# Optimization experiments

Hardware: AMD Instinct MI355X
Metric: run time of the kernel (lower is better)

## Reference

```python
import jax, jax.numpy as jnp
import numpy as np
from jax import lax

B, IMG, CIN, C, HEADS, K = 2, 112, 64, 256, 8, 3  # kernel_size[0]=3 used by hatt1
HD = C // HEADS


def layer_norm(x, w, b, eps=1e-5):
    mu = jnp.mean(x, axis=-1, keepdims=True)
    var = jnp.mean((x - mu) ** 2, axis=-1, keepdims=True)
    return (x - mu) / jnp.sqrt(var + eps) * w + b


def conv3x3(x, w, b):
    # x: (B,Cin,H,W), w: (Cout,Cin,3,3) -- stride 1, pad 1 (OverlapPatchEmbed patchsize=3)
    y = lax.conv_general_dilated(x, w, (1, 1), ((1, 1), (1, 1)),
                                 dimension_numbers=('NCHW', 'OIHW', 'NCHW'))
    return y + b[None, :, None, None]


def nat_cross_attention(q_in, kv_in, wq, bq, wkv, bkv, rpb, wp, bp, heads=HEADS, k=K):
    # NATTEN-style 2D neighborhood attention with separate query / key-value maps.
    Bb, H, W, Cc = q_in.shape
    hd = Cc // heads
    scale = hd ** -0.5
    q = (q_in @ wq + bq).reshape(Bb, H, W, heads, hd) * scale
    kv = (kv_in @ wkv + bkv).reshape(Bb, H, W, 2, heads, hd)
    kk, v = kv[:, :, :, 0], kv[:, :, :, 1]
    half = k // 2
    # border-clamped window starts -> every pixel attends to a full k x k window
    si = jnp.clip(jnp.arange(H) - half, 0, H - k)  # (H,)
    sj = jnp.clip(jnp.arange(W) - half, 0, W - k)  # (W,)
    nbi = si[:, None] + jnp.arange(k)  # (H,k) neighbor rows
    nbj = sj[:, None] + jnp.arange(k)  # (W,k) neighbor cols

    def gather(t):  # t: (B,H,W,heads,hd) -> (B,H,W,heads,k*k,hd)
        g = t[:, nbi]            # (B,H,k,W,heads,hd)
        g = g[:, :, :, nbj]      # (B,H,k,W,k,heads,hd)
        return jnp.transpose(g, (0, 1, 3, 5, 2, 4, 6)).reshape(Bb, H, W, heads, k * k, hd)

    kg, vg = gather(kk), gather(v)
    logits = jnp.einsum('bijhd,bijhnd->bijhn', q, kg)
    # relative position bias: rpb (heads, 2k-1, 2k-1)
    pi = jnp.arange(H) - si  # query position inside its window, 0..k-1
    pj = jnp.arange(W) - sj
    idx_i = jnp.arange(k)[None, :] - pi[:, None] + (k - 1)  # (H,k) in [0, 2k-2]
    idx_j = jnp.arange(k)[None, :] - pj[:, None] + (k - 1)  # (W,k)
    bias = rpb[:, idx_i]           # (heads,H,k,2k-1)
    bias = bias[:, :, :, idx_j]    # (heads,H,k,W,k)
    bias = jnp.transpose(bias, (1, 3, 0, 2, 4)).reshape(H, W, heads, k * k)
    attn = jax.nn.softmax(logits + bias, axis=-1)
    out = jnp.einsum('bijhn,bijhnd->bijhd', attn, vg).reshape(Bb, H, W, Cc)
    return out @ wp + bp


def setup_inputs() -> dict:
    key = jax.random.key(0)
    ks = jax.random.split(key, 24)
    std = 0.02
    inp = {
        'xq': jax.random.normal(ks[0], (B, CIN, IMG, IMG), jnp.float32),
        'xkv': jax.random.normal(ks[1], (B, CIN, IMG, IMG), jnp.float32),
        'conv1_w': jax.random.normal(ks[2], (C, CIN, 3, 3), jnp.float32) * std,
        'conv1_b': jnp.zeros((C,), jnp.float32),
        'conv3_w': jax.random.normal(ks[3], (C, CIN, 3, 3), jnp.float32) * std,
        'conv3_b': jnp.zeros((C,), jnp.float32),
        'ln1_w': jnp.ones((C,), jnp.float32), 'ln1_b': jnp.zeros((C,), jnp.float32),
        'ln10_w': jnp.ones((C,), jnp.float32), 'ln10_b': jnp.zeros((C,), jnp.float32),
        'ln3_w': jnp.ones((C,), jnp.float32), 'ln3_b': jnp.zeros((C,), jnp.float32),
        'wq': jax.random.normal(ks[4], (C, C), jnp.float32) * std,
        'bq': jnp.zeros((C,), jnp.float32),
        'wkv': jax.random.normal(ks[5], (C, 2 * C), jnp.float32) * std,
        'bkv': jnp.zeros((2 * C,), jnp.float32),
        'rpb': jax.random.normal(ks[6], (HEADS, 2 * K - 1, 2 * K - 1), jnp.float32) * std,
        'wp': jax.random.normal(ks[7], (C, C), jnp.float32) * std,
        'bp': jnp.zeros((C,), jnp.float32),
        'fc1_w': jax.random.normal(ks[8], (C, 2 * C), jnp.float32) * std,
        'fc1_b': jnp.zeros((2 * C,), jnp.float32),
        'fc2_w': jax.random.normal(ks[9], (2 * C, C), jnp.float32) * std,
        'fc2_b': jnp.zeros((C,), jnp.float32),
    }
    return inp


def reference(xq, xkv, conv1_w, conv1_b, conv3_w, conv3_b, ln1_w, ln1_b, ln10_w, ln10_b,
              ln3_w, ln3_b, wq, bq, wkv, bkv, rpb, wp, bp, fc1_w, fc1_b, fc2_w, fc2_b):
    # patch embeds (stride-1 3x3 conv, pad 1), channels-last maps (B,H,W,C)
    x1 = jnp.transpose(conv3x3(xq, conv1_w, conv1_b), (0, 2, 3, 1))
    x3 = jnp.transpose(conv3x3(xkv, conv3_w, conv3_b), (0, 2, 3, 1))
    qn = layer_norm(x1, ln1_w, ln1_b)    # norm1(x_embedding1)
    kvn = layer_norm(x1, ln10_w, ln10_b)  # norm1_0(x_embedding1)
    att1 = nat_cross_attention(qn, kvn, wq, bq, wkv, bkv, rpb, wp, bp)
    att = att1 + x3  # drop_path is identity at inference
    h = layer_norm(att, ln3_w, ln3_b)
    m = jax.nn.gelu(h @ fc1_w + fc1_b, approximate=False) @ fc2_w + fc2_b
    x = m + att
    return jnp.transpose(x, (0, 3, 1, 2))  # (B,C,H,W)
```

## Files before the change

### kernel.cpp

```cpp
#include <hip/hip_runtime.h>
#include <math.h>

#define IMG 112
#define CIN 64
#define CH 256
#define PADW 114
#define IMG2 12544
#define NPIX 25088

typedef __bf16 bf16;
typedef __bf16 bf16x4 __attribute__((ext_vector_type(4)));
typedef __bf16 bf16x8 __attribute__((ext_vector_type(8)));
typedef float f32x4 __attribute__((ext_vector_type(4)));

__device__ __forceinline__ void gld_lds16(const void* g, void* l) {
    __builtin_amdgcn_global_load_lds(
        (const __attribute__((address_space(1))) void*)g,
        (__attribute__((address_space(3))) void*)l,
        16, 0, 0);
}

#define VMCNT0() asm volatile("s_waitcnt vmcnt(0)" ::: "memory")
#define BAR() __builtin_amdgcn_s_barrier()

__global__ __launch_bounds__(256) void pad_nhwc_kernel(const float* __restrict__ in, bf16* __restrict__ out) {
    int bi = blockIdx.x;
    int b = bi / IMG, i = bi % IMG;
    __shared__ float lds[CIN * 113];
    const float* src = in + (size_t)b * CIN * IMG2 + (size_t)i * IMG;
    for (int t = threadIdx.x; t < CIN * IMG; t += 256) {
        int ci = t / IMG, j = t - ci * IMG;
        lds[ci * 113 + j] = src[(size_t)ci * IMG2 + j];
    }
    __syncthreads();
    bf16* dst = out + (((size_t)(b * PADW + (i + 1)) * PADW) + 1) * CIN;
    for (int t = threadIdx.x; t < CIN * IMG; t += 256) {
        int j = t / CIN, ci = t - j * CIN;
        dst[(size_t)j * CIN + ci] = (bf16)lds[ci * 113 + j];
    }
}

__global__ __launch_bounds__(256) void convw_kernel(const float* __restrict__ w1, const float* __restrict__ w2,
                                                    bf16* __restrict__ o1, bf16* __restrict__ o2) {
    int idx = blockIdx.x * 256 + threadIdx.x;
    if (idx >= CH * 576) return;
    int co = idx / 576, r = idx - co * 576;
    int tap = r >> 6, ci = r & 63;
    int src = co * 576 + ci * 9 + tap;
    o1[idx] = (bf16)w1[src];
    o2[idx] = (bf16)w2[src];
}

__global__ __launch_bounds__(256) void transw_kernel(const float* __restrict__ in, bf16* __restrict__ out,
                                                     int K, int N, float scale) {
    int idx = blockIdx.x * 256 + threadIdx.x;
    if (idx >= N * K) return;
    int n = idx / K, k = idx - n * K;
    out[idx] = (bf16)(in[(size_t)k * N + n] * scale);
}

template <int NOUT>
__global__ __launch_bounds__(256) void ln_kernel(
    const float* __restrict__ x,
    const float* __restrict__ w0, const float* __restrict__ b0, bf16* __restrict__ o0,
    const float* __restrict__ w1, const float* __restrict__ b1, bf16* __restrict__ o1) {
    int row = blockIdx.x * 4 + (threadIdx.x >> 6);
    int lane = threadIdx.x & 63;
    const float* xr = x + (size_t)row * CH + lane * 4;
    f32x4 v = *(const f32x4*)xr;
    float s = v[0] + v[1] + v[2] + v[3];
    float ss = v[0] * v[0] + v[1] * v[1] + v[2] * v[2] + v[3] * v[3];
#pragma unroll
    for (int off = 32; off > 0; off >>= 1) {
        s += __shfl_xor(s, off);
        ss += __shfl_xor(ss, off);
    }
    float mean = s * (1.0f / CH);
    float rstd = rsqrtf(ss * (1.0f / CH) - mean * mean + 1e-5f);
    int c = lane * 4;
    {
        f32x4 w = *(const f32x4*)(w0 + c);
        f32x4 bb = *(const f32x4*)(b0 + c);
        bf16x4 o;
#pragma unroll
        for (int e = 0; e < 4; ++e) o[e] = (bf16)((v[e] - mean) * rstd * w[e] + bb[e]);
        *(bf16x4*)(o0 + (size_t)row * CH + c) = o;
    }
    if (NOUT == 2) {
        f32x4 w = *(const f32x4*)(w1 + c);
        f32x4 bb = *(const f32x4*)(b1 + c);
        bf16x4 o;
#pragma unroll
        for (int e = 0; e < 4; ++e) o[e] = (bf16)((v[e] - mean) * rstd * w[e] + bb[e]);
        *(bf16x4*)(o1 + (size_t)row * CH + c) = o;
    }
}

template <int AMODE, int EPI>
__global__ __launch_bounds__(256, 5) void gemm_kernel(
    const bf16* __restrict__ A, const bf16* __restrict__ Bt,
    const float* __restrict__ bias, float biasScale,
    const float* __restrict__ res,
    float* __restrict__ outf, bf16* __restrict__ outb,
    int N, int K) {
    __shared__ __align__(16) bf16 As[2][64 * 64];
    __shared__ __align__(16) bf16 Bs[2][64 * 64];
    const int tid = threadIdx.x;
    const int wave = tid >> 6, lane = tid & 63;
    const int m0 = blockIdx.x * 64, n0 = blockIdx.y * 64;
    const int wm = wave >> 1, wn = wave & 1;
    const int fr = lane & 15, fq = lane >> 4;

    const int srow = (lane >> 3);
    const int swzc = (lane & 7) ^ srow;
    const int scol = swzc * 8;

    const bf16* aptr[2];
    const bf16* bptr[2];
#pragma unroll
    for (int q = 0; q < 2; ++q) {
        int arow = m0 + wave * 16 + q * 8 + srow;
        if (AMODE == 1) {
            int b = arow / IMG2;
            int rem = arow - b * IMG2;
            int i = rem / IMG, j = rem - i * IMG;
            aptr[q] = A + ((size_t)((b * PADW + i) * PADW + j)) * CIN + scol;
        } else {
            aptr[q] = A + (size_t)arow * K + scol;
        }
        bptr[q] = Bt + (size_t)(n0 + wave * 16 + q * 8 + srow) * K + scol;
    }

    auto STAGE = [&](int bufi, int kt) {
        int aoff;
        if (AMODE == 1) {
            int di = kt / 3, dj = kt - di * 3;
            aoff = (di * PADW + dj) * CIN;
        } else {
            aoff = kt * 64;
        }
        int boff = kt * 64;
        gld_lds16(aptr[0] + aoff, &As[bufi][(wave * 16 + 0) * 64]);
        gld_lds16(aptr[1] + aoff, &As[bufi][(wave * 16 + 8) * 64]);
        gld_lds16(bptr[0] + boff, &Bs[bufi][(wave * 16 + 0) * 64]);
        gld_lds16(bptr[1] + boff, &Bs[bufi][(wave * 16 + 8) * 64]);
    };

    f32x4 acc[2][2] = {};
    const int sw = fr & 7;
    const int aR[2] = { (wm * 32 + fr) * 64, (wm * 32 + 16 + fr) * 64 };
    const int bR[2] = { (wn * 32 + fr) * 64, (wn * 32 + 16 + fr) * 64 };

    auto COMPUTE = [&](int bufi) {
#pragma unroll
        for (int ks = 0; ks < 2; ++ks) {
            int ch = (ks * 4 + fq) ^ sw;
            bf16x8 af[2], bv[2];
#pragma unroll
            for (int mi = 0; mi < 2; ++mi) af[mi] = *(const bf16x8*)&As[bufi][aR[mi] + ch * 8];
#pragma unroll
            for (int ni = 0; ni < 2; ++ni) bv[ni] = *(const bf16x8*)&Bs[bufi][bR[ni] + ch * 8];
#pragma unroll
            for (int mi = 0; mi < 2; ++mi)
#pragma unroll
                for (int ni = 0; ni < 2; ++ni)
                    acc[mi][ni] = __builtin_amdgcn_mfma_f32_16x16x32_bf16(af[mi], bv[ni], acc[mi][ni], 0, 0, 0);
        }
    };

    const int nk = K >> 6;
    STAGE(0, 0);
    VMCNT0();
    BAR();
    int cur = 0;
    for (int kt = 0; kt < nk - 1; ++kt) {
        STAGE(cur ^ 1, kt + 1);
        COMPUTE(cur);
        VMCNT0();
        BAR();
        cur ^= 1;
    }
    COMPUTE(cur);

#pragma unroll
    for (int mi = 0; mi < 2; ++mi) {
#pragma unroll
        for (int ni = 0; ni < 2; ++ni) {
            int col = n0 + wn * 32 + ni * 16 + fr;
            float bv = (EPI & 1) ? bias[col] * biasScale : 0.0f;
#pragma unroll
            for (int r = 0; r < 4; ++r) {
                int prow = m0 + wm * 32 + mi * 16 + fq * 4 + r;
                float x = acc[mi][ni][r] + bv;
                if (EPI & 2) x = 0.5f * x * (1.0f + erff(x * 0.70710678118f));
                if (EPI & 4) x += res[(size_t)prow * N + col];
                if (EPI & 8) outf[(size_t)prow * N + col] = x;
                if (EPI & 16) outb[(size_t)prow * N + col] = (bf16)x;
                if (EPI & 32) {
                    int b = prow / IMG2;
                    int rem = prow - b * IMG2;
                    int ii = rem / IMG, jj = rem - ii * IMG;
                    outf[(((size_t)b * CH + col) * IMG + ii) * IMG + jj] = x;
                }
            }
        }
    }
}

__global__ __launch_bounds__(256) void attn_kernel(const bf16* __restrict__ q, const bf16* __restrict__ kv,
                                                   const float* __restrict__ rpb, bf16* __restrict__ out) {
    int idx = blockIdx.x * 256 + threadIdx.x;
    int h = idx & 7, p = idx >> 3;
    int b = p / IMG2;
    int rem = p - b * IMG2;
    int i = rem / IMG, j = rem - i * IMG;
    int si = i - 1; if (si < 0) si = 0; if (si > IMG - 3) si = IMG - 3;
    int sj = j - 1; if (sj < 0) sj = 0; if (sj > IMG - 3) sj = IMG - 3;
    int pi = i - si, pj = j - sj;

    float qv[32];
    {
        const bf16x8* qp = (const bf16x8*)(q + (size_t)p * CH + h * 32);
#pragma unroll
        for (int g = 0; g < 4; ++g) {
            bf16x8 t = qp[g];
#pragma unroll
            for (int e = 0; e < 8; ++e) qv[g * 8 + e] = (float)t[e];
        }
    }
    float logits[9];
#pragma unroll
    for (int a = 0; a < 3; ++a) {
#pragma unroll
        for (int bb = 0; bb < 3; ++bb) {
            int pn = (b * IMG + (si + a)) * IMG + (sj + bb);
            const bf16x8* kp = (const bf16x8*)(kv + (size_t)pn * 512 + h * 32);
            float s = 0.0f;
#pragma unroll
            for (int g = 0; g < 4; ++g) {
                bf16x8 t = kp[g];
#pragma unroll
                for (int e = 0; e < 8; ++e) s += qv[g * 8 + e] * (float)t[e];
            }
            logits[a * 3 + bb] = s + rpb[(h * 5 + (a - pi + 2)) * 5 + (bb - pj + 2)];
        }
    }
    float mx = logits[0];
#pragma unroll
    for (int n = 1; n < 9; ++n) mx = fmaxf(mx, logits[n]);
    float den = 0.0f;
#pragma unroll
    for (int n = 0; n < 9; ++n) { logits[n] = expf(logits[n] - mx); den += logits[n]; }
    float inv = 1.0f / den;
    float o[32] = {};
#pragma unroll
    for (int a = 0; a < 3; ++a) {
#pragma unroll
        for (int bb = 0; bb < 3; ++bb) {
            int pn = (b * IMG + (si + a)) * IMG + (sj + bb);
            float wgt = logits[a * 3 + bb] * inv;
            const bf16x8* vp = (const bf16x8*)(kv + (size_t)pn * 512 + 256 + h * 32);
#pragma unroll
            for (int g = 0; g < 4; ++g) {
                bf16x8 t = vp[g];
#pragma unroll
                for (int e = 0; e < 8; ++e) o[g * 8 + e] += wgt * (float)t[e];
            }
        }
    }
    bf16* op = out + (size_t)p * CH + h * 32;
#pragma unroll
    for (int g = 0; g < 4; ++g) {
        bf16x8 t;
#pragma unroll
        for (int e = 0; e < 8; ++e) t[e] = (bf16)o[g * 8 + e];
        *(bf16x8*)(op + g * 8) = t;
    }
}

extern "C" void kernel_launch(void* const* d_in, const int* in_sizes, int n_in,
                              void* d_out, int out_size, void* d_ws, size_t ws_size,
                              hipStream_t stream) {
    (void)in_sizes; (void)n_in; (void)out_size; (void)ws_size;
    const float* xq    = (const float*)d_in[0];
    const float* xkv   = (const float*)d_in[1];
    const float* c1w   = (const float*)d_in[2];
    const float* c1b   = (const float*)d_in[3];
    const float* c3w   = (const float*)d_in[4];
    const float* c3b   = (const float*)d_in[5];
    const float* ln1w  = (const float*)d_in[6];
    const float* ln1b  = (const float*)d_in[7];
    const float* ln10w = (const float*)d_in[8];
    const float* ln10b = (const float*)d_in[9];
    const float* ln3w  = (const float*)d_in[10];
    const float* ln3b  = (const float*)d_in[11];
    const float* wq    = (const float*)d_in[12];
    const float* bq    = (const float*)d_in[13];
    const float* wkv   = (const float*)d_in[14];
    const float* bkv   = (const float*)d_in[15];
    const float* rpb   = (const float*)d_in[16];
    const float* wp    = (const float*)d_in[17];
    const float* bp    = (const float*)d_in[18];
    const float* f1w   = (const float*)d_in[19];
    const float* f1b   = (const float*)d_in[20];
    const float* f2w   = (const float*)d_in[21];
    const float* f2b   = (const float*)d_in[22];
    float* out = (float*)d_out;

    char* ws = (char*)d_ws;
    bf16*  PADQ  = (bf16*)(ws + 0);
    bf16*  PADKV = (bf16*)(ws + 3326976);
    bf16*  CW1   = (bf16*)(ws + 6653952);
    bf16*  CW2   = (bf16*)(ws + 6948864);
    bf16*  WQT   = (bf16*)(ws + 7243776);
    bf16*  WKVT  = (bf16*)(ws + 7374848);
    bf16*  WPT   = (bf16*)(ws + 7636992);
    bf16*  WF1   = (bf16*)(ws + 7768064);
    bf16*  WF2   = (bf16*)(ws + 8030208);
    float* X1    = (float*)(ws + 8292352);
    bf16*  KV    = (bf16*)(ws + 8292352);
    float* X3    = (float*)(ws + 33982464);
    bf16*  QN    = (bf16*)(ws + 59672576);
    bf16*  M1    = (bf16*)(ws + 59672576);
    bf16*  KVN   = (bf16*)(ws + 72517632);
    bf16*  Q     = (bf16*)(ws + 85362688);
    bf16*  H     = (bf16*)(ws + 85362688);
    bf16*  AO    = (bf16*)(ws + 98207744);
    float* ATT   = (float*)(ws + 111052800);

    const float SC = 0.17677669529663687f;

    hipMemsetAsync(PADQ, 0, 6653952, stream);
    pad_nhwc_kernel<<<224, 256, 0, stream>>>(xq, PADQ);
    pad_nhwc_kernel<<<224, 256, 0, stream>>>(xkv, PADKV);
    convw_kernel<<<576, 256, 0, stream>>>(c1w, c3w, CW1, CW2);
    transw_kernel<<<256, 256, 0, stream>>>(wq, WQT, 256, 256, SC);
    transw_kernel<<<512, 256, 0, stream>>>(wkv, WKVT, 256, 512, 1.0f);
    transw_kernel<<<256, 256, 0, stream>>>(wp, WPT, 256, 256, 1.0f);
    transw_kernel<<<512, 256, 0, stream>>>(f1w, WF1, 256, 512, 1.0f);
    transw_kernel<<<512, 256, 0, stream>>>(f2w, WF2, 512, 256, 1.0f);

    dim3 g4(392, 4), g8(392, 8);
    gemm_kernel<1, 1 | 8><<<g4, 256, 0, stream>>>(PADQ, CW1, c1b, 1.0f, nullptr, X1, nullptr, 256, 576);
    gemm_kernel<1, 1 | 8><<<g4, 256, 0, stream>>>(PADKV, CW2, c3b, 1.0f, nullptr, X3, nullptr, 256, 576);
    ln_kernel<2><<<6272, 256, 0, stream>>>(X1, ln1w, ln1b, QN, ln10w, ln10b, KVN);
    gemm_kernel<0, 1 | 16><<<g4, 256, 0, stream>>>(QN, WQT, bq, SC, nullptr, nullptr, Q, 256, 256);
    gemm_kernel<0, 1 | 16><<<g8, 256, 0, stream>>>(KVN, WKVT, bkv, 1.0f, nullptr, nullptr, KV, 512, 256);
    attn_kernel<<<784, 256, 0, stream>>>(Q, KV, rpb, AO);
    gemm_kernel<0, 1 | 4 | 8><<<g4, 256, 0, stream>>>(AO, WPT, bp, 1.0f, X3, ATT, nullptr, 256, 256);
    ln_kernel<1><<<6272, 256, 0, stream>>>(ATT, ln3w, ln3b, H, nullptr, nullptr, nullptr);
    gemm_kernel<0, 1 | 2 | 16><<<g8, 256, 0, stream>>>(H, WF1, f1b, 1.0f, nullptr, nullptr, M1, 512, 256);
    gemm_kernel<0, 1 | 4 | 32><<<g4, 256, 0, stream>>>(M1, WF2, f2b, 1.0f, ATT, out, nullptr, 256, 512);
}
```

Before: 298.3 us.

## Fuse prep kernels, widen GEMM tiles to full rows, fold LayerNorms into GEMM epilogues

All weight and input prep launches are merged into a single kernel, and the memset is replaced by writing only the padding borders. The GEMM now computes 64x256 tiles so each block holds full channel rows, which lets both LayerNorms run in the epilogues through LDS row reductions, and the NCHW output is written with vectorized stores through an LDS transpose. Intermediate activations such as X3 and ATT are stored in bf16 instead of fp32, cutting memory traffic but adding rounding error. The change removes several launches and full fp32 round trips, but the larger tile uses 80KB LDS per block and needs more accumulator registers, which lowers occupancy.

```diff
diff --git a/kernel.cpp b/kernel.cpp
--- a/kernel.cpp
+++ b/kernel.cpp
@@ -7,9 +7,9 @@
 #define PADW 114
 #define IMG2 12544
 #define NPIX 25088
+#define SCQ 0.17677669529663687f
 
 typedef __bf16 bf16;
-typedef __bf16 bf16x4 __attribute__((ext_vector_type(4)));
 typedef __bf16 bf16x8 __attribute__((ext_vector_type(8)));
 typedef float f32x4 __attribute__((ext_vector_type(4)));
 
@@ -19,104 +19,97 @@
         (__attribute__((address_space(3))) void*)l,
         16, 0, 0);
 }
-
 #define VMCNT0() asm volatile("s_waitcnt vmcnt(0)" ::: "memory")
 #define BAR() __builtin_amdgcn_s_barrier()
 
-__global__ __launch_bounds__(256) void pad_nhwc_kernel(const float* __restrict__ in, bf16* __restrict__ out) {
-    int bi = blockIdx.x;
-    int b = bi / IMG, i = bi % IMG;
+__global__ __launch_bounds__(256) void prep_kernel(
+    const float* __restrict__ xq, const float* __restrict__ xkv,
+    bf16* __restrict__ padq, bf16* __restrict__ padkv,
+    const float* __restrict__ c1w, const float* __restrict__ c3w,
+    bf16* __restrict__ cw1, bf16* __restrict__ cw2,
+    const float* __restrict__ wq, bf16* __restrict__ wqt,
+    const float* __restrict__ wkv, bf16* __restrict__ wkvt,
+    const float* __restrict__ wp, bf16* __restrict__ wpt,
+    const float* __restrict__ f1w, bf16* __restrict__ wf1,
+    const float* __restrict__ f2w, bf16* __restrict__ wf2) {
+    int bid = blockIdx.x, tid = threadIdx.x;
     __shared__ float lds[CIN * 113];
-    const float* src = in + (size_t)b * CIN * IMG2 + (size_t)i * IMG;
-    for (int t = threadIdx.x; t < CIN * IMG; t += 256) {
-        int ci = t / IMG, j = t - ci * IMG;
-        lds[ci * 113 + j] = src[(size_t)ci * IMG2 + j];
-    }
-    __syncthreads();
-    bf16* dst = out + (((size_t)(b * PADW + (i + 1)) * PADW) + 1) * CIN;
-    for (int t = threadIdx.x; t < CIN * IMG; t += 256) {
-        int j = t / CIN, ci = t - j * CIN;
-        dst[(size_t)j * CIN + ci] = (bf16)lds[ci * 113 + j];
-    }
-}
-
-__global__ __launch_bounds__(256) void convw_kernel(const float* __restrict__ w1, const float* __restrict__ w2,
-                                                    bf16* __restrict__ o1, bf16* __restrict__ o2) {
-    int idx = blockIdx.x * 256 + threadIdx.x;
-    if (idx >= CH * 576) return;
-    int co = idx / 576, r = idx - co * 576;
-    int tap = r >> 6, ci = r & 63;
-    int src = co * 576 + ci * 9 + tap;
-    o1[idx] = (bf16)w1[src];
-    o2[idx] = (bf16)w2[src];
-}
-
-__global__ __launch_bounds__(256) void transw_kernel(const float* __restrict__ in, bf16* __restrict__ out,
-                                                     int K, int N, float scale) {
-    int idx = blockIdx.x * 256 + threadIdx.x;
-    if (idx >= N * K) return;
-    int n = idx / K, k = idx - n * K;
-    out[idx] = (bf16)(in[(size_t)k * N + n] * scale);
-}
-
-template <int NOUT>
-__global__ __launch_bounds__(256) void ln_kernel(
-    const float* __restrict__ x,
-    const float* __restrict__ w0, const float* __restrict__ b0, bf16* __restrict__ o0,
-    const float* __restrict__ w1, const float* __restrict__ b1, bf16* __restrict__ o1) {
-    int row = blockIdx.x * 4 + (threadIdx.x >> 6);
-    int lane = threadIdx.x & 63;
-    const float* xr = x + (size_t)row * CH + lane * 4;
-    f32x4 v = *(const f32x4*)xr;
-    float s = v[0] + v[1] + v[2] + v[3];
-    float ss = v[0] * v[0] + v[1] * v[1] + v[2] * v[2] + v[3] * v[3];
-#pragma unroll
-    for (int off = 32; off > 0; off >>= 1) {
-        s += __shfl_xor(s, off);
-        ss += __shfl_xor(ss, off);
-    }
-    float mean = s * (1.0f / CH);
-    float rstd = rsqrtf(ss * (1.0f / CH) - mean * mean + 1e-5f);
-    int c = lane * 4;
-    {
-        f32x4 w = *(const f32x4*)(w0 + c);
-        f32x4 bb = *(const f32x4*)(b0 + c);
-        bf16x4 o;
-#pragma unroll
-        for (int e = 0; e < 4; ++e) o[e] = (bf16)((v[e] - mean) * rstd * w[e] + bb[e]);
-        *(bf16x4*)(o0 + (size_t)row * CH + c) = o;
-    }
-    if (NOUT == 2) {
-        f32x4 w = *(const f32x4*)(w1 + c);
-        f32x4 bb = *(const f32x4*)(b1 + c);
-        bf16x4 o;
-#pragma unroll
-        for (int e = 0; e < 4; ++e) o[e] = (bf16)((v[e] - mean) * rstd * w[e] + bb[e]);
-        *(bf16x4*)(o1 + (size_t)row * CH + c) = o;
-    }
-}
-
-template <int AMODE, int EPI>
-__global__ __launch_bounds__(256, 5) void gemm_kernel(
-    const bf16* __restrict__ A, const bf16* __restrict__ Bt,
-    const float* __restrict__ bias, float biasScale,
-    const float* __restrict__ res,
-    float* __restrict__ outf, bf16* __restrict__ outb,
-    int N, int K) {
-    __shared__ __align__(16) bf16 As[2][64 * 64];
-    __shared__ __align__(16) bf16 Bs[2][64 * 64];
+    if (bid < 448) {
+        const float* in = (bid < 224) ? xq : xkv;
+        bf16* out = (bid < 224) ? padq : padkv;
+        int bi = (bid < 224) ? bid : bid - 224;
+        int b = bi / IMG, i = bi % IMG;
+        const float* src = in + (size_t)b * CIN * IMG2 + (size_t)i * IMG;
+        for (int t = tid; t < CIN * IMG; t += 256) {
+            int ci = t / IMG, j = t - ci * IMG;
+            lds[ci * 113 + j] = src[(size_t)ci * IMG2 + j];
+        }
+        __syncthreads();
+        bf16* dst = out + (((size_t)(b * PADW + (i + 1)) * PADW) + 1) * CIN;
+        for (int t = tid; t < CIN * IMG; t += 256) {
+            int j = t / CIN, ci = t - j * CIN;
+            dst[(size_t)j * CIN + ci] = (bf16)lds[ci * 113 + j];
+        }
+        bf16* rowbase = out + ((size_t)(b * PADW + (i + 1)) * PADW) * CIN;
+        if (tid < 128) rowbase[(tid >> 6 ? 113 * CIN : 0) + (tid & 63)] = (bf16)0.0f;
+        if (i == 0)
+            for (int t = tid; t < PADW * CIN; t += 256)
+                out[((size_t)(b * PADW + 0) * PADW) * CIN + t] = (bf16)0.0f;
+        if (i == IMG - 1)
+            for (int t = tid; t < PADW * CIN; t += 256)
+                out[((size_t)(b * PADW + 113) * PADW) * CIN + t] = (bf16)0.0f;
+    } else if (bid < 1024) {
+        int idx = (bid - 448) * 256 + tid;
+        int co = idx / 576, r = idx - co * 576;
+        int tap = r >> 6, ci = r & 63;
+        int src = co * 576 + ci * 9 + tap;
+        cw1[idx] = (bf16)c1w[src];
+        cw2[idx] = (bf16)c3w[src];
+    } else {
+        int off = (bid - 1024) * 256 + tid;
+        const float* in; bf16* out; int K, N; float sc = 1.0f; int base;
+        if (off < 65536)       { in = wq;  out = wqt;  K = 256; N = 256; sc = SCQ; base = 0; }
+        else if (off < 196608) { in = wkv; out = wkvt; K = 256; N = 512; base = 65536; }
+        else if (off < 262144) { in = wp;  out = wpt;  K = 256; N = 256; base = 196608; }
+        else if (off < 393216) { in = f1w; out = wf1;  K = 256; N = 512; base = 262144; }
+        else                   { in = f2w; out = wf2;  K = 512; N = 256; base = 393216; }
+        int idx = off - base;
+        int n = idx / K, k = idx - n * K;
+        out[idx] = (bf16)(in[(size_t)k * N + n] * sc);
+    }
+}
+
+#define M_DENSE 0
+#define M_LN2   1
+#define M_WPLN  2
+#define M_GELU  3
+#define M_NCHW  4
+
+template <int AMODE, int MODE>
+__device__ __forceinline__ void gemm_core(
+    char* sm,
+    const bf16* __restrict__ A, const bf16* __restrict__ B,
+    const float* __restrict__ bias, float bscale,
+    const bf16* __restrict__ res,
+    bf16* __restrict__ out0, int ldo0,
+    bf16* __restrict__ out1, float* __restrict__ outf,
+    const float* __restrict__ lnw0, const float* __restrict__ lnb0,
+    const float* __restrict__ lnw1, const float* __restrict__ lnb1,
+    int K) {
+    bf16* As = (bf16*)sm;
+    bf16* Bs = (bf16*)(sm + 16384);
+    float* lnb = (float*)sm;
+    float* T = (float*)(sm + 2048);
+
     const int tid = threadIdx.x;
     const int wave = tid >> 6, lane = tid & 63;
-    const int m0 = blockIdx.x * 64, n0 = blockIdx.y * 64;
+    const int m0 = blockIdx.x * 64;
     const int wm = wave >> 1, wn = wave & 1;
     const int fr = lane & 15, fq = lane >> 4;
-
-    const int srow = (lane >> 3);
-    const int swzc = (lane & 7) ^ srow;
-    const int scol = swzc * 8;
+    const int srow = lane >> 3;
+    const int scol = ((lane & 7) ^ srow) * 8;
 
     const bf16* aptr[2];
-    const bf16* bptr[2];
 #pragma unroll
     for (int q = 0; q < 2; ++q) {
         int arow = m0 + wave * 16 + q * 8 + srow;
@@ -128,42 +121,38 @@
         } else {
             aptr[q] = A + (size_t)arow * K + scol;
         }
-        bptr[q] = Bt + (size_t)(n0 + wave * 16 + q * 8 + srow) * K + scol;
-    }
-
-    auto STAGE = [&](int bufi, int kt) {
-        int aoff;
-        if (AMODE == 1) {
-            int di = kt / 3, dj = kt - di * 3;
-            aoff = (di * PADW + dj) * CIN;
-        } else {
-            aoff = kt * 64;
-        }
+    }
+    const bf16* bptr0 = B + (size_t)(wave * 64 + srow) * K + scol;
+
+    auto STAGE = [&](int bi, int kt) {
+        int aoff = (AMODE == 1) ? ((kt / 3) * PADW + (kt - (kt / 3) * 3)) * CIN : kt * 64;
         int boff = kt * 64;
-        gld_lds16(aptr[0] + aoff, &As[bufi][(wave * 16 + 0) * 64]);
-        gld_lds16(aptr[1] + aoff, &As[bufi][(wave * 16 + 8) * 64]);
-        gld_lds16(bptr[0] + boff, &Bs[bufi][(wave * 16 + 0) * 64]);
-        gld_lds16(bptr[1] + boff, &Bs[bufi][(wave * 16 + 8) * 64]);
+        bf16* ad = As + bi * 4096 + (wave * 16) * 64;
+        gld_lds16(aptr[0] + aoff, ad);
+        gld_lds16(aptr[1] + aoff, ad + 8 * 64);
+        bf16* bd = Bs + bi * 16384 + (wave * 64) * 64;
+#pragma unroll
+        for (int u = 0; u < 8; ++u)
+            gld_lds16(bptr0 + (size_t)u * 8 * K + boff, bd + u * 8 * 64);
     };
 
-    f32x4 acc[2][2] = {};
-    const int sw = fr & 7;
-    const int aR[2] = { (wm * 32 + fr) * 64, (wm * 32 + 16 + fr) * 64 };
-    const int bR[2] = { (wn * 32 + fr) * 64, (wn * 32 + 16 + fr) * 64 };
-
-    auto COMPUTE = [&](int bufi) {
+    f32x4 acc[2][8] = {};
+    auto COMPUTE = [&](int bi) {
+        const bf16* ab = As + bi * 4096;
+        const bf16* bb = Bs + bi * 16384;
 #pragma unroll
         for (int ks = 0; ks < 2; ++ks) {
-            int ch = (ks * 4 + fq) ^ sw;
-            bf16x8 af[2], bv[2];
-#pragma unroll
-            for (int mi = 0; mi < 2; ++mi) af[mi] = *(const bf16x8*)&As[bufi][aR[mi] + ch * 8];
-#pragma unroll
-            for (int ni = 0; ni < 2; ++ni) bv[ni] = *(const bf16x8*)&Bs[bufi][bR[ni] + ch * 8];
+            int ch = ((ks * 4 + fq) ^ (fr & 7)) * 8;
+            bf16x8 af[2];
+#pragma unroll
+            for (int mi = 0; mi < 2; ++mi) af[mi] = *(const bf16x8*)&ab[(wm * 32 + mi * 16 + fr) * 64 + ch];
+            bf16x8 bv[8];
+#pragma unroll
+            for (int ni = 0; ni < 8; ++ni) bv[ni] = *(const bf16x8*)&bb[(wn * 128 + ni * 16 + fr) * 64 + ch];
 #pragma unroll
             for (int mi = 0; mi < 2; ++mi)
 #pragma unroll
-                for (int ni = 0; ni < 2; ++ni)
+                for (int ni = 0; ni < 8; ++ni)
                     acc[mi][ni] = __builtin_amdgcn_mfma_f32_16x16x32_bf16(af[mi], bv[ni], acc[mi][ni], 0, 0, 0);
         }
     };
@@ -182,29 +171,196 @@
     }
     COMPUTE(cur);
 
-#pragma unroll
-    for (int mi = 0; mi < 2; ++mi) {
-#pragma unroll
-        for (int ni = 0; ni < 2; ++ni) {
-            int col = n0 + wn * 32 + ni * 16 + fr;
-            float bv = (EPI & 1) ? bias[col] * biasScale : 0.0f;
+    float bvv[8];
+#pragma unroll
+    for (int ni = 0; ni < 8; ++ni) bvv[ni] = bias[wn * 128 + ni * 16 + fr] * bscale;
+#pragma unroll
+    for (int mi = 0; mi < 2; ++mi)
+#pragma unroll
+        for (int ni = 0; ni < 8; ++ni)
 #pragma unroll
             for (int r = 0; r < 4; ++r) {
-                int prow = m0 + wm * 32 + mi * 16 + fq * 4 + r;
-                float x = acc[mi][ni][r] + bv;
-                if (EPI & 2) x = 0.5f * x * (1.0f + erff(x * 0.70710678118f));
-                if (EPI & 4) x += res[(size_t)prow * N + col];
-                if (EPI & 8) outf[(size_t)prow * N + col] = x;
-                if (EPI & 16) outb[(size_t)prow * N + col] = (bf16)x;
-                if (EPI & 32) {
-                    int b = prow / IMG2;
-                    int rem = prow - b * IMG2;
-                    int ii = rem / IMG, jj = rem - ii * IMG;
-                    outf[(((size_t)b * CH + col) * IMG + ii) * IMG + jj] = x;
-                }
-            }
-        }
-    }
+                float x = acc[mi][ni][r] + bvv[ni];
+                if (MODE == M_WPLN) {
+                    int prow = m0 + wm * 32 + mi * 16 + fq * 4 + r;
+                    int col = wn * 128 + ni * 16 + fr;
+                    x += (float)res[(size_t)prow * 256 + col];
+                }
+                if (MODE == M_GELU) x = 0.5f * x * (1.0f + erff(x * 0.70710678118f));
+                acc[mi][ni][r] = x;
+            }
+
+    float mean_[2][4], rstd_[2][4];
+    if (MODE == M_LN2 || MODE == M_WPLN) {
+        BAR();
+#pragma unroll
+        for (int mi = 0; mi < 2; ++mi)
+#pragma unroll
+            for (int r = 0; r < 4; ++r) {
+                float s = 0.0f, ss = 0.0f;
+#pragma unroll
+                for (int ni = 0; ni < 8; ++ni) {
+                    float x = acc[mi][ni][r];
+                    s += x; ss += x * x;
+                }
+#pragma unroll
+                for (int msk = 1; msk <= 8; msk <<= 1) {
+                    s += __shfl_xor(s, msk);
+                    ss += __shfl_xor(ss, msk);
+                }
+                if (fr == 0) {
+                    int row = wm * 32 + mi * 16 + fq * 4 + r;
+                    lnb[wn * 128 + row] = s;
+                    lnb[wn * 128 + 64 + row] = ss;
+                }
+            }
+        BAR();
+#pragma unroll
+        for (int mi = 0; mi < 2; ++mi)
+#pragma unroll
+            for (int r = 0; r < 4; ++r) {
+                int row = wm * 32 + mi * 16 + fq * 4 + r;
+                float s = lnb[row] + lnb[128 + row];
+                float ss = lnb[64 + row] + lnb[192 + row];
+                float mean = s * (1.0f / CH);
+                float var = ss * (1.0f / CH) - mean * mean;
+                mean_[mi][r] = mean;
+                rstd_[mi][r] = rsqrtf(var + 1e-5f);
+            }
+    } else {
+        BAR();
+    }
+
+#pragma unroll
+    for (int mi = 0; mi < 2; ++mi)
+#pragma unroll
+        for (int ni = 0; ni < 8; ++ni)
+#pragma unroll
+            for (int r = 0; r < 4; ++r) {
+                int row = wm * 32 + mi * 16 + fq * 4 + r;
+                int col = wn * 128 + ni * 16 + fr;
+                float x = acc[mi][ni][r];
+                if (MODE == M_LN2) x = (x - mean_[mi][r]) * rstd_[mi][r];
+                T[row * 257 + col] = x;
+            }
+    BAR();
+
+    if (MODE == M_NCHW) {
+        int c = tid;
+        int b = m0 / IMG2, p0 = m0 - b * IMG2;
+        float* outp = outf + ((size_t)(b * CH + c)) * IMG2 + p0;
+        const bf16* rp = res + (size_t)m0 * 256 + c;
+#pragma unroll
+        for (int g = 0; g < 16; ++g) {
+            f32x4 v;
+#pragma unroll
+            for (int e = 0; e < 4; ++e)
+                v[e] = T[(g * 4 + e) * 257 + c] + (float)rp[(size_t)(g * 4 + e) * 256];
+            *(f32x4*)(outp + g * 4) = v;
+        }
+    } else {
+        int row = tid & 63, qd = tid >> 6;
+        int cb = qd * 64;
+        if (MODE == M_DENSE || MODE == M_GELU) {
+            bf16* op = out0 + (size_t)(m0 + row) * ldo0 + cb;
+#pragma unroll
+            for (int g = 0; g < 8; ++g) {
+                bf16x8 o;
+#pragma unroll
+                for (int e = 0; e < 8; ++e) o[e] = (bf16)T[row * 257 + cb + g * 8 + e];
+                *(bf16x8*)(op + g * 8) = o;
+            }
+        } else if (MODE == M_LN2) {
+            bf16* op0 = out0 + (size_t)(m0 + row) * 256 + cb;
+            bf16* op1 = out1 + (size_t)(m0 + row) * 256 + cb;
+#pragma unroll
+            for (int g = 0; g < 8; ++g) {
+                bf16x8 o0, o1;
+#pragma unroll
+                for (int e = 0; e < 8; ++e) {
+                    int c = cb + g * 8 + e;
+                    float xh = T[row * 257 + c];
+                    o0[e] = (bf16)(xh * lnw0[c] + lnb0[c]);
+                    o1[e] = (bf16)(xh * lnw1[c] + lnb1[c]);
+                }
+                *(bf16x8*)(op0 + g * 8) = o0;
+                *(bf16x8*)(op1 + g * 8) = o1;
+            }
+        } else if (MODE == M_WPLN) {
+            float s = lnb[row] + lnb[128 + row];
+            float ss = lnb[64 + row] + lnb[192 + row];
+            float mean = s * (1.0f / CH);
+            float rstd = rsqrtf(ss * (1.0f / CH) - mean * mean + 1e-5f);
+            bf16* op0 = out0 + (size_t)(m0 + row) * 256 + cb;
+            bf16* op1 = out1 + (size_t)(m0 + row) * 256 + cb;
+#pragma unroll
+            for (int g = 0; g < 8; ++g) {
+                bf16x8 o0, o1;
+#pragma unroll
+                for (int e = 0; e < 8; ++e) {
+                    int c = cb + g * 8 + e;
+                    float x = T[row * 257 + c];
+                    o0[e] = (bf16)x;
+                    o1[e] = (bf16)((x - mean) * rstd * lnw0[c] + lnb0[c]);
+                }
+                *(bf16x8*)(op0 + g * 8) = o0;
+                *(bf16x8*)(op1 + g * 8) = o1;
+            }
+        }
+    }
+}
+
+__global__ __launch_bounds__(256) void conv_kernel(
+    const bf16* padq, const bf16* padkv, const bf16* cw1, const bf16* cw2,
+    const float* c1b, const float* c3b,
+    bf16* qn, bf16* kvn, bf16* x3,
+    const float* l1w, const float* l1b, const float* l10w, const float* l10b) {
+    __shared__ char sm[81920];
+    if (blockIdx.y == 0)
+        gemm_core<1, M_LN2>(sm, padq, cw1, c1b, 1.0f, nullptr, qn, 256, kvn, nullptr,
+                            l1w, l1b, l10w, l10b, 576);
+    else
+        gemm_core<1, M_DENSE>(sm, padkv, cw2, c3b, 1.0f, nullptr, x3, 256, nullptr, nullptr,
+                              nullptr, nullptr, nullptr, nullptr, 576);
+}
+
+__global__ __launch_bounds__(256) void qkv_kernel(
+    const bf16* qnp, const bf16* kvnp, const bf16* wqt, const bf16* wkvt,
+    const float* bq, const float* bkv, bf16* q, bf16* kv) {
+    __shared__ char sm[81920];
+    int by = blockIdx.y;
+    const bf16* A = by ? kvnp : qnp;
+    const bf16* B = by ? (wkvt + (size_t)(by - 1) * 65536) : wqt;
+    const float* bias = by ? (bkv + (by - 1) * 256) : bq;
+    float bsc = by ? 1.0f : SCQ;
+    bf16* out = by ? (kv + (by - 1) * 256) : q;
+    int ldo = by ? 512 : 256;
+    gemm_core<0, M_DENSE>(sm, A, B, bias, bsc, nullptr, out, ldo, nullptr, nullptr,
+                          nullptr, nullptr, nullptr, nullptr, 256);
+}
+
+__global__ __launch_bounds__(256) void wp_kernel(
+    const bf16* ao, const bf16* wpt, const float* bp, const bf16* x3,
+    bf16* att, bf16* h, const float* l3w, const float* l3b) {
+    __shared__ char sm[81920];
+    gemm_core<0, M_WPLN>(sm, ao, wpt, bp, 1.0f, x3, att, 256, h, nullptr,
+                         l3w, l3b, nullptr, nullptr, 256);
+}
+
+__global__ __launch_bounds__(256) void fc1_kernel(
+    const bf16* h, const bf16* wf1, const float* f1b, bf16* m1) {
+    __shared__ char sm[81920];
+    int by = blockIdx.y;
+    gemm_core<0, M_GELU>(sm, h, wf1 + (size_t)by * 65536, f1b + by * 256, 1.0f, nullptr,
+                         m1 + by * 256, 512, nullptr, nullptr,
+                         nullptr, nullptr, nullptr, nullptr, 256);
+}
+
+__global__ __launch_bounds__(256) void fc2_kernel(
+    const bf16* m1, const bf16* wf2, const float* f2b, const bf16* att, float* out) {
+    __shared__ char sm[81920];
+    gemm_core<0, M_NCHW>(sm, m1, wf2, f2b, 1.0f, att, nullptr, 0, nullptr, out,
+                         nullptr, nullptr, nullptr, nullptr, 512);
 }
 
 __global__ __launch_bounds__(256) void attn_kernel(const bf16* __restrict__ q, const bf16* __restrict__ kv,
@@ -308,47 +464,32 @@
     float* out = (float*)d_out;
 
     char* ws = (char*)d_ws;
-    bf16*  PADQ  = (bf16*)(ws + 0);
-    bf16*  PADKV = (bf16*)(ws + 3326976);
-    bf16*  CW1   = (bf16*)(ws + 6653952);
-    bf16*  CW2   = (bf16*)(ws + 6948864);
-    bf16*  WQT   = (bf16*)(ws + 7243776);
-    bf16*  WKVT  = (bf16*)(ws + 7374848);
-    bf16*  WPT   = (bf16*)(ws + 7636992);
-    bf16*  WF1   = (bf16*)(ws + 7768064);
-    bf16*  WF2   = (bf16*)(ws + 8030208);
-    float* X1    = (float*)(ws + 8292352);
-    bf16*  KV    = (bf16*)(ws + 8292352);
-    float* X3    = (float*)(ws + 33982464);
-    bf16*  QN    = (bf16*)(ws + 59672576);
-    bf16*  M1    = (bf16*)(ws + 59672576);
-    bf16*  KVN   = (bf16*)(ws + 72517632);
-    bf16*  Q     = (bf16*)(ws + 85362688);
-    bf16*  H     = (bf16*)(ws + 85362688);
-    bf16*  AO    = (bf16*)(ws + 98207744);
-    float* ATT   = (float*)(ws + 111052800);
-
-    const float SC = 0.17677669529663687f;
-
-    hipMemsetAsync(PADQ, 0, 6653952, stream);
-    pad_nhwc_kernel<<<224, 256, 0, stream>>>(xq, PADQ);
-    pad_nhwc_kernel<<<224, 256, 0, stream>>>(xkv, PADKV);
-    convw_kernel<<<576, 256, 0, stream>>>(c1w, c3w, CW1, CW2);
-    transw_kernel<<<256, 256, 0, stream>>>(wq, WQT, 256, 256, SC);
-    transw_kernel<<<512, 256, 0, stream>>>(wkv, WKVT, 256, 512, 1.0f);
-    transw_kernel<<<256, 256, 0, stream>>>(wp, WPT, 256, 256, 1.0f);
-    transw_kernel<<<512, 256, 0, stream>>>(f1w, WF1, 256, 512, 1.0f);
-    transw_kernel<<<512, 256, 0, stream>>>(f2w, WF2, 512, 256, 1.0f);
-
-    dim3 g4(392, 4), g8(392, 8);
-    gemm_kernel<1, 1 | 8><<<g4, 256, 0, stream>>>(PADQ, CW1, c1b, 1.0f, nullptr, X1, nullptr, 256, 576);
-    gemm_kernel<1, 1 | 8><<<g4, 256, 0, stream>>>(PADKV, CW2, c3b, 1.0f, nullptr, X3, nullptr, 256, 576);
-    ln_kernel<2><<<6272, 256, 0, stream>>>(X1, ln1w, ln1b, QN, ln10w, ln10b, KVN);
-    gemm_kernel<0, 1 | 16><<<g4, 256, 0, stream>>>(QN, WQT, bq, SC, nullptr, nullptr, Q, 256, 256);
-    gemm_kernel<0, 1 | 16><<<g8, 256, 0, stream>>>(KVN, WKVT, bkv, 1.0f, nullptr, nullptr, KV, 512, 256);
+    bf16* PADQ  = (bf16*)(ws + 0);
+    bf16* PADKV = (bf16*)(ws + 3326976);
+    bf16* CW1   = (bf16*)(ws + 6653952);
+    bf16* CW2   = (bf16*)(ws + 6948864);
+    bf16* WQT   = (bf16*)(ws + 7243776);
+    bf16* WKVT  = (bf16*)(ws + 7374848);
+    bf16* WPT   = (bf16*)(ws + 7636992);
+    bf16* WF1   = (bf16*)(ws + 7768064);
+    bf16* WF2   = (bf16*)(ws + 8030208);
+    bf16* QN    = (bf16*)(ws + 8292352);
+    bf16* KVN   = (bf16*)(ws + 21137408);
+    bf16* Q     = (bf16*)(ws + 33982464);
+    bf16* KV    = (bf16*)(ws + 46827520);
+    bf16* AO    = (bf16*)(ws + 72517632);
+    bf16* X3    = (bf16*)(ws + 85362688);
+    bf16* ATT   = (bf16*)(ws + 98207744);
+    bf16* H     = (bf16*)(ws + 111052800);
+    bf16* M1    = (bf16*)(ws + 123897856);
+
+    prep_kernel<<<3072, 256, 0, stream>>>(xq, xkv, PADQ, PADKV, c1w, c3w, CW1, CW2,
+                                          wq, WQT, wkv, WKVT, wp, WPT, f1w, WF1, f2w, WF2);
+    conv_kernel<<<dim3(392, 2), 256, 0, stream>>>(PADQ, PADKV, CW1, CW2, c1b, c3b,
+                                                  QN, KVN, X3, ln1w, ln1b, ln10w, ln10b);
+    qkv_kernel<<<dim3(392, 3), 256, 0, stream>>>(QN, KVN, WQT, WKVT, bq, bkv, Q, KV);
     attn_kernel<<<784, 256, 0, stream>>>(Q, KV, rpb, AO);
-    gemm_kernel<0, 1 | 4 | 8><<<g4, 256, 0, stream>>>(AO, WPT, bp, 1.0f, X3, ATT, nullptr, 256, 256);
-    ln_kernel<1><<<6272, 256, 0, stream>>>(ATT, ln3w, ln3b, H, nullptr, nullptr, nullptr);
-    gemm_kernel<0, 1 | 2 | 16><<<g8, 256, 0, stream>>>(H, WF1, f1b, 1.0f, nullptr, nullptr, M1, 512, 256);
-    gemm_kernel<0, 1 | 4 | 32><<<g4, 256, 0, stream>>>(M1, WF2, f2b, 1.0f, ATT, out, nullptr, 256, 512);
-}
+    wp_kernel<<<392, 256, 0, stream>>>(AO, WPT, bp, X3, ATT, H, ln3w, ln3b);
+    fc1_kernel<<<dim3(392, 2), 256, 0, stream>>>(H, WF1, f1b, M1);
+    fc2_kernel<<<392, 256, 0, stream>>>(M1, WF2, f2b, ATT, out);
+}
```

Measured after the change: 291.1 us. 2.4% less time.
